# Optimization experiments

Hardware: AMD Instinct MI355X
Metric: run time of the kernel (lower is better)

The kernel has to match this reference:

```python
import jax, jax.numpy as jnp
import numpy as np

APERTURE = 128
LN_EPS = 1e-6

def _layer_norm(y, g, b):
    mu = jnp.mean(y, axis=-1, keepdims=True)
    var = jnp.var(y, axis=-1, keepdims=True)
    return (y - mu) / jnp.sqrt(var + LN_EPS) * g + b

def setup_inputs() -> dict:
    key = jax.random.key(0)
    ks = jax.random.split(key, 12)
    B, S, D = 4, 4096, 1024
    gain = np.sqrt(2.0)
    xav = lambda k, fan_out, fan_in: jax.random.uniform(
        k, (fan_out, fan_in), jnp.float32,
        -gain * np.sqrt(6.0 / (fan_in + fan_out)), gain * np.sqrt(6.0 / (fan_in + fan_out)))
    return {
        "x": jax.random.normal(ks[0], (B, S, D), jnp.float32),
        "Wq": xav(ks[1], D, D),
        "Wk": xav(ks[2], D, D),
        "Wv": xav(ks[3], D, D),
        "Wo": xav(ks[4], D, D),
        "k1_w": xav(ks[5], D, D),
        "k1_b": jnp.full((D,), 0.1, jnp.float32),
        "k2_w": xav(ks[6], 1, D),
        "k2_b": jnp.full((1,), 0.1, jnp.float32),
        "ln_g": jnp.ones((D,), jnp.float32),
        "ln_b": jnp.zeros((D,), jnp.float32),
    }

def reference(x, Wq, Wk, Wv, Wo, k1_w, k1_b, k2_w, k2_b, ln_g, ln_b):
    B, S, D = x.shape
    scale = jnp.float32(1.0 / np.sqrt(D))
    neg_inf = jnp.float32(-np.inf)

    Q = x @ Wq.T  # [B,S,D]
    K = x @ Wk.T
    V = x @ Wv.T

    e = jnp.einsum('bsd,btd->bst', Q, K) * scale  # [B,S,S]

    # ignore_self: -inf on the diagonal
    i = jnp.arange(S)[:, None]
    j = jnp.arange(S)[None, :]
    e = jnp.where(i == j, neg_inf, e)

    # banded aperture mask: tril(e, ap) * triu(e, -ap); zeros of the product -> -inf
    d = j - i
    scope = jnp.where(d <= APERTURE, e, 0.0) * jnp.where(d >= -APERTURE, e, 0.0)
    e = jnp.where(scope == 0.0, neg_inf, e)

    alpha = jax.nn.softmax(e, axis=2)
    c = jnp.einsum('bst,btd->bsd', alpha, V)
    c = c @ Wo.T

    y = c + x
    y = _layer_norm(y, ln_g, ln_b)
    y = jax.nn.relu(y @ k1_w.T + k1_b)
    y = _layer_norm(y, ln_g, ln_b)
    y = jax.nn.sigmoid(y @ k2_w.T + k2_b)  # [B,S,1]
    return y.reshape(B, S)
```

## Files before the change

### kernel.cpp

```cpp
#include <hip/hip_runtime.h>
#include <math.h>

#define DD 1024
#define SS 4096
#define AP 128
#define LN_EPS 1e-6f
#define BK 32
#define BAND 384

typedef __bf16 bf16;
typedef __attribute__((ext_vector_type(4))) __bf16 bf16x4;
typedef __attribute__((ext_vector_type(8))) __bf16 bf16x8;
typedef __attribute__((ext_vector_type(4))) float f32x4;

#define GLOAD_LDS16(g, l)                                                   \
    __builtin_amdgcn_global_load_lds(                                        \
        (const __attribute__((address_space(1))) void*)(g),                  \
        (__attribute__((address_space(3))) void*)(l), 16, 0, 0)

__global__ __launch_bounds__(256) void prep_all(const float* __restrict__ x,
                                                const float* __restrict__ Wq,
                                                const float* __restrict__ Wk,
                                                const float* __restrict__ Wv,
                                                const float* __restrict__ Wo,
                                                const float* __restrict__ k1w,
                                                const float* __restrict__ k1b,
                                                const float* __restrict__ lng,
                                                const float* __restrict__ lnb,
                                                bf16* __restrict__ xb,
                                                bf16* __restrict__ Wob,
                                                bf16* __restrict__ k1g,
                                                bf16* __restrict__ Wtb,
                                                float* __restrict__ u1,
                                                float* __restrict__ c1b) {
    __shared__ float tile[64][65];
    const int bid = blockIdx.x;
    const int tid = threadIdx.x;
    if (bid < 16384) {
        const int i = (bid * 256 + tid) * 4;
        const float4 a = *(const float4*)(x + i);
        bf16x4 o;
        o[0] = (__bf16)a.x; o[1] = (__bf16)a.y; o[2] = (__bf16)a.z; o[3] = (__bf16)a.w;
        *(bf16x4*)(xb + i) = o;
        return;
    }
    if (bid < 18432) {
        const int b2 = bid - 16384;
        const int sel = b2 >> 10;
        const int bb = b2 & 1023;
        const float* s = sel ? k1w : Wo;
        bf16* d = sel ? k1g : Wob;
        const int i = (bb * 256 + tid) * 4;
        float4 a = *(const float4*)(s + i);
        if (sel) {
            const float4 g4 = *(const float4*)(lng + (i & (DD - 1)));
            a.x *= g4.x; a.y *= g4.y; a.z *= g4.z; a.w *= g4.w;
        }
        bf16x4 o;
        o[0] = (__bf16)a.x; o[1] = (__bf16)a.y; o[2] = (__bf16)a.z; o[3] = (__bf16)a.w;
        *(bf16x4*)(d + i) = o;
        return;
    }
    if (bid < 19200) {
        const int t = bid - 18432;
        const int tz = t >> 8;
        const int tb_ = t & 255;
        const float* in = (tz == 0) ? Wq : (tz == 1) ? Wk : Wv;
        bf16* out = Wtb + ((size_t)tz << 20);
        const int r0 = (tb_ >> 4) * 64, c0 = (tb_ & 15) * 64;
        const int lr = tid >> 4;
        const int lc = (tid & 15) * 4;
#pragma unroll
        for (int rr = 0; rr < 4; rr++) {
            const int row = lr + rr * 16;
            const float4 v = *(const float4*)(in + (size_t)(r0 + row) * DD + c0 + lc);
            tile[row][lc] = v.x; tile[row][lc + 1] = v.y;
            tile[row][lc + 2] = v.z; tile[row][lc + 3] = v.w;
        }
        __syncthreads();
#pragma unroll
        for (int rr = 0; rr < 4; rr++) {
            const int row = lr + rr * 16;
            bf16x4 o;
            o[0] = (__bf16)tile[lc + 0][row];
            o[1] = (__bf16)tile[lc + 1][row];
            o[2] = (__bf16)tile[lc + 2][row];
            o[3] = (__bf16)tile[lc + 3][row];
            *(bf16x4*)(out + (size_t)(c0 + row) * DD + r0 + lc) = o;
        }
        return;
    }
    const int pv = bid - 19200;
    const int lane = tid & 63, wave = tid >> 6;
    const int n = pv * 4 + wave;
    const float* row = k1w + (size_t)n * DD + lane * 16;
    float su = 0.f, sb = 0.f;
#pragma unroll
    for (int q = 0; q < 4; q++) {
        const float4 a = *(const float4*)(row + q * 4);
        const float4 g4 = *(const float4*)(lng + lane * 16 + q * 4);
        const float4 b4 = *(const float4*)(lnb + lane * 16 + q * 4);
        su += a.x * g4.x + a.y * g4.y + a.z * g4.z + a.w * g4.w;
        sb += a.x * b4.x + a.y * b4.y + a.z * b4.z + a.w * b4.w;
    }
#pragma unroll
    for (int off = 32; off > 0; off >>= 1) {
        su += __shfl_xor(su, off);
        sb += __shfl_xor(sb, off);
    }
    if (lane == 0) {
        u1[n] = su;
        c1b[n] = sb + k1b[n];
    }
}

__global__ __launch_bounds__(256) void gemm_pair(const bf16* __restrict__ A0,
                                                 const bf16* __restrict__ W0,
                                                 bf16* __restrict__ O0,
                                                 const bf16* __restrict__ A1,
                                                 const bf16* __restrict__ W1,
                                                 bf16* __restrict__ O1) {
    const bf16* A = blockIdx.z ? A1 : A0;
    const bf16* W = blockIdx.z ? W1 : W0;
    bf16* O = blockIdx.z ? O1 : O0;
    __shared__ bf16 As[128 * BK];
    __shared__ bf16 Bs[128 * BK];
    const int tid = threadIdx.x;
    const int lane = tid & 63;
    const int wave = tid >> 6;
    const int wm = wave & 1;
    const int wn = wave >> 1;
    const int m0 = blockIdx.y * 128;
    const int n0 = blockIdx.x * 128;

    const int c = wave * 64 + lane;
    const int ar = c >> 2;
    const int ac = (c & 3) << 3;
    char* AsB = (char*)As;
    char* BsB = (char*)Bs;
    const int lr = lane & 15;
    const int lk = (lane >> 4) << 3;

    f32x4 acc[4][4] = {};

    for (int kt = 0; kt < DD; kt += BK) {
        const bf16* ga0 = A + (size_t)(m0 + ar) * DD + kt + ac;
        const bf16* gb0 = W + (size_t)(n0 + ar) * DD + kt + ac;
        GLOAD_LDS16(ga0, AsB + wave * 1024);
        GLOAD_LDS16(ga0 + (size_t)64 * DD, AsB + 4096 + wave * 1024);
        GLOAD_LDS16(gb0, BsB + wave * 1024);
        GLOAD_LDS16(gb0 + (size_t)64 * DD, BsB + 4096 + wave * 1024);
        __syncthreads();

        bf16x8 af[4], bfr[4];
#pragma unroll
        for (int i = 0; i < 4; i++)
            af[i] = *(const bf16x8*)&As[(wm * 64 + i * 16 + lr) * BK + lk];
#pragma unroll
        for (int j = 0; j < 4; j++)
            bfr[j] = *(const bf16x8*)&Bs[(wn * 64 + j * 16 + lr) * BK + lk];
#pragma unroll
        for (int i = 0; i < 4; i++)
#pragma unroll
            for (int j = 0; j < 4; j++)
                acc[i][j] = __builtin_amdgcn_mfma_f32_16x16x32_bf16(af[i], bfr[j], acc[i][j], 0, 0, 0);
        __syncthreads();
    }

#pragma unroll
    for (int i = 0; i < 4; i++) {
        const int row = m0 + wm * 64 + i * 16 + ((lane >> 4) << 2);
#pragma unroll
        for (int j = 0; j < 4; j++) {
            const int col = n0 + wn * 64 + j * 16 + (lane & 15);
#pragma unroll
            for (int rr = 0; rr < 4; rr++)
                O[(size_t)(row + rr) * DD + col] = (__bf16)acc[i][j][rr];
        }
    }
}


#define KL_STAGE_A(tt, hh, bb)                                               \
    {                                                                        \
        const bf16* gp_ = Aop + gofsA + (tt) * 64 + (hh) * 32;               \
        GLOAD_LDS16(gp_, smem + (bb) + (hh) * 16384 + ldsW);                 \
        GLOAD_LDS16(gp_ + (size_t)128 * DD,                                  \
                    smem + (bb) + (hh) * 16384 + 8192 + ldsW);               \
    }
#define KL_STAGE_B(tt, hh, bb)                                               \
    {                                                                        \
        const bf16* gp_ = Bop + gofsB + (tt) * 64 + (hh) * 32;               \
        GLOAD_LDS16(gp_, smem + (bb) + 32768 + (hh) * 16384 + ldsW);         \
        GLOAD_LDS16(gp_ + (size_t)128 * DD,                                  \
                    smem + (bb) + 32768 + (hh) * 16384 + 8192 + ldsW);       \
    }
#define KL_READS_A(ks, mh)                                                   \
    af[0] = *(const bf16x8*)(sA + bufo + (ks) * 16384 + (mh) * 4096);        \
    af[1] = *(const bf16x8*)(sA + bufo + (ks) * 16384 + (mh) * 4096 + 1024); \
    af[2] = *(const bf16x8*)(sA + bufo + (ks) * 16384 + (mh) * 4096 + 2048); \
    af[3] = *(const bf16x8*)(sA + bufo + (ks) * 16384 + (mh) * 4096 + 3072);
#define KL_READS_B(ks)                                                       \
    bfr[0] = *(const bf16x8*)(sB + bufo + (ks) * 16384);                     \
    bfr[1] = *(const bf16x8*)(sB + bufo + (ks) * 16384 + 1024);              \
    bfr[2] = *(const bf16x8*)(sB + bufo + (ks) * 16384 + 2048);              \
    bfr[3] = *(const bf16x8*)(sB + bufo + (ks) * 16384 + 3072);
#define KL_MFMA4(I, MH)                                                      \
    acc[(MH) * 4 + I][0] = __builtin_amdgcn_mfma_f32_16x16x32_bf16(af[I], bfr[0], acc[(MH) * 4 + I][0], 0, 0, 0); \
    acc[(MH) * 4 + I][1] = __builtin_amdgcn_mfma_f32_16x16x32_bf16(af[I], bfr[1], acc[(MH) * 4 + I][1], 0, 0, 0); \
    acc[(MH) * 4 + I][2] = __builtin_amdgcn_mfma_f32_16x16x32_bf16(af[I], bfr[2], acc[(MH) * 4 + I][2], 0, 0, 0); \
    acc[(MH) * 4 + I][3] = __builtin_amdgcn_mfma_f32_16x16x32_bf16(af[I], bfr[3], acc[(MH) * 4 + I][3], 0, 0, 0);
#define KL_MFMA16(MH)                                                        \
    __builtin_amdgcn_s_setprio(1);                                           \
    KL_MFMA4(0, MH) KL_MFMA4(1, MH) KL_MFMA4(2, MH) KL_MFMA4(3, MH)          \
    __builtin_amdgcn_s_setprio(0);
#define KL_BARRIER(N) asm volatile("s_waitcnt vmcnt(" #N ")\n\ts_barrier" ::: "memory")

__device__ __forceinline__ void kloop256(const bf16* __restrict__ Aop,
                                         const bf16* __restrict__ Bop,
                                         const int m0, const int n0,
                                         char* smem, f32x4 (&acc)[8][4],
                                         const int tid, const int lane,
                                         const int wave, const int wm, const int wn) {
    const int grow = tid >> 2;
    const int gslot = (tid & 3) ^ ((tid >> 3) & 3);
    const size_t gofsA = (size_t)(m0 + grow) * DD + gslot * 8;
    const size_t gofsB = (size_t)(n0 + grow) * DD + gslot * 8;
    const int ldsW = wave * 1024;
    const int sxo = (((lane >> 4) ^ ((lane >> 1) & 3)) << 4);
    const char* sA = smem + wm * 8192 + (lane & 15) * 64 + sxo;
    const char* sB = smem + 32768 + wn * 4096 + (lane & 15) * 64 + sxo;

    bf16x8 af[4], bfr[4];

    KL_STAGE_A(0, 0, 0) KL_STAGE_B(0, 0, 0)
    KL_STAGE_A(0, 1, 0) KL_STAGE_B(0, 1, 0)
    KL_STAGE_A(1, 0, 65536) KL_STAGE_B(1, 0, 65536)

    int bufo = 0;
    for (int t = 0; t < 15; t++) {
        const int nb = bufo ^ 65536;
        KL_BARRIER(8);
        KL_READS_A(0, 0) KL_READS_B(0)
        KL_STAGE_A(t + 1, 1, nb)
        KL_MFMA16(0)
        KL_READS_A(0, 1)
        KL_STAGE_B(t + 1, 1, nb)
        KL_MFMA16(1)
        KL_BARRIER(8);
        KL_READS_A(1, 0) KL_READS_B(1)
        if (t < 14) { KL_STAGE_A(t + 2, 0, bufo) }
        KL_MFMA16(0)
        KL_READS_A(1, 1)
        if (t < 14) { KL_STAGE_B(t + 2, 0, bufo) }
        KL_MFMA16(1)
        bufo = nb;
    }
    KL_BARRIER(4);
    KL_READS_A(0, 0) KL_READS_B(0)
    KL_MFMA16(0)
    KL_READS_A(0, 1)
    KL_MFMA16(1)
    KL_BARRIER(0);
    KL_READS_A(1, 0) KL_READS_B(1)
    KL_MFMA16(0)
    KL_READS_A(1, 1)
    KL_MFMA16(1)
}

__global__ __launch_bounds__(512) void gemm_uv(const bf16* __restrict__ xb,
                                               const bf16* __restrict__ Gt,
                                               const bf16* __restrict__ W2,
                                               bf16* __restrict__ Ub,
                                               bf16* __restrict__ Vt2) {
    __shared__ char smem[131072];
    const int s = blockIdx.x;
    const int half = s >> 8;
    const int sh = s & 255;
    const int p = (sh & 7) | ((sh >> 5) << 3);
    const int q = (sh >> 3) & 3;
    const bf16* A;
    const bf16* W;
    bf16* O;
    int m0, n0;
    size_t ldo;
    if (half == 0) {
        A = xb; W = Gt; O = Ub;
        m0 = p * 256; n0 = q * 256; ldo = DD;
    } else {
        A = W2; W = xb; O = Vt2;
        m0 = q * 256; n0 = p * 256; ldo = (size_t)4 * SS;
    }
    const int tid = threadIdx.x;
    const int lane = tid & 63;
    const int wave = tid >> 6;
    const int wm = wave & 1;
    const int wn = wave >> 1;

    f32x4 acc[8][4] = {};
    kloop256(A, W, m0, n0, smem, acc, tid, lane, wave, wm, wn);

#pragma unroll
    for (int a = 0; a < 8; a++) {
        const int row = m0 + wm * 128 + a * 16 + ((lane >> 4) << 2);
#pragma unroll
        for (int j = 0; j < 4; j++) {
            const int col = n0 + wn * 64 + j * 16 + (lane & 15);
#pragma unroll
            for (int rr = 0; rr < 4; rr++)
                O[(size_t)(row + rr) * ldo + col] = (__bf16)acc[a][j][rr];
        }
    }
}

__global__ __launch_bounds__(512) void gemm_k1(const bf16* __restrict__ T,
                                               const bf16* __restrict__ k1g,
                                               const float* __restrict__ part_t,
                                               const float* __restrict__ u1,
                                               const float* __restrict__ c1b,
                                               const float* __restrict__ lng,
                                               const float* __restrict__ k2w,
                                               float* __restrict__ part_h) {
    __shared__ char smem[131072];
    __shared__ float lmu[256], lrs[256];
    const int m0 = blockIdx.x * 256;
    const int n0 = blockIdx.y * 256;
    const int tid = threadIdx.x;
    const int lane = tid & 63;
    const int wave = tid >> 6;
    const int wm = wave & 1;
    const int wn = wave >> 1;

    if (tid < 256) {
        const float* p = part_t + (size_t)(m0 + tid) * 32;
        float s1 = 0.f, s2 = 0.f;
#pragma unroll
        for (int s = 0; s < 8; s++) {
            const float4 v = *(const float4*)(p + s * 4);
            s1 += v.x + v.z;
            s2 += v.y + v.w;
        }
        const float m = s1 * (1.f / DD);
        lmu[tid] = m;
        lrs[tid] = rsqrtf(s2 * (1.f / DD) - m * m + LN_EPS);
    }
    __syncthreads();

    f32x4 acc[8][4] = {};
    kloop256(T, k1g, m0, n0, smem, acc, tid, lane, wave, wm, wn);

    float u1v[4], cbv[4], ugv[4];
#pragma unroll
    for (int j = 0; j < 4; j++) {
        const int col = n0 + wn * 64 + j * 16 + (lane & 15);
        u1v[j] = u1[col];
        cbv[j] = c1b[col];
        ugv[j] = lng[col] * k2w[col];
    }
    const int strip = blockIdx.y * 4 + wn;
#pragma unroll
    for (int a = 0; a < 8; a++) {
#pragma unroll
        for (int rr = 0; rr < 4; rr++) {
            const int lrow = wm * 128 + a * 16 + ((lane >> 4) << 2) + rr;
            const int row = m0 + lrow;
            const float mr = lmu[lrow], rs = lrs[lrow];
            float s1 = 0.f, s2 = 0.f, s3 = 0.f;
#pragma unroll
            for (int j = 0; j < 4; j++) {
                const float v = rs * (acc[a][j][rr] - mr * u1v[j]) + cbv[j];
                const float h = fmaxf(v, 0.f);
                s1 += h; s2 += h * h; s3 += h * ugv[j];
            }
#pragma unroll
            for (int off = 8; off > 0; off >>= 1) {
                s1 += __shfl_xor(s1, off);
                s2 += __shfl_xor(s2, off);
                s3 += __shfl_xor(s3, off);
            }
            if ((lane & 15) == 0) {
                float* p = part_h + (size_t)row * 48 + strip * 3;
                p[0] = s1; p[1] = s2; p[2] = s3;
            }
        }
    }
}

#define SP_STAGE(tt, bb)                                                      \
    {                                                                         \
        const int kt_ = (tt) * 64;                                            \
        GLOAD_LDS16(U + gofsA + kt_, smem + (bb) + ldsWA);                    \
        GLOAD_LDS16(X + gofsB + kt_, smem + (bb) + 8192 + ldsW);              \
        GLOAD_LDS16(X + gofsB + (long)128 * DD + kt_, smem + (bb) + 16384 + ldsW); \
        GLOAD_LDS16(X + gofsB + (long)256 * DD + kt_, smem + (bb) + 24576 + ldsW); \
        GLOAD_LDS16(X + gofsB + kt_ + 32, smem + (bb) + 32768 + ldsW);        \
        GLOAD_LDS16(X + gofsB + (long)128 * DD + kt_ + 32, smem + (bb) + 40960 + ldsW); \
        GLOAD_LDS16(X + gofsB + (long)256 * DD + kt_ + 32, smem + (bb) + 49152 + ldsW); \
    }
#define SP_READS(bb)                                                          \
    _Pragma("unroll") for (int i_ = 0; i_ < 2; i_++) {                        \
        a0[i_] = *(const bf16x8*)(sA + (bb) + wm * 2048 + i_ * 1024);         \
        a1[i_] = *(const bf16x8*)(sA + (bb) + 4096 + wm * 2048 + i_ * 1024);  \
    }                                                                         \
    _Pragma("unroll") for (int j_ = 0; j_ < 6; j_++) {                        \
        b0[j_] = *(const bf16x8*)(sB + (bb) + wn * 6144 + j_ * 1024);         \
        b1[j_] = *(const bf16x8*)(sB + (bb) + 24576 + wn * 6144 + j_ * 1024); \
    }
#define SP_MFMA(AR, BR)                                                       \
    __builtin_amdgcn_s_setprio(1);                                            \
    _Pragma("unroll") for (int i_ = 0; i_ < 2; i_++)                          \
        _Pragma("unroll") for (int j_ = 0; j_ < 6; j_++)                      \
            acc[i_][j_] = __builtin_amdgcn_mfma_f32_16x16x32_bf16(AR[i_], BR[j_], acc[i_][j_], 0, 0, 0); \
    __builtin_amdgcn_s_setprio(0);
#define SP_LGBAR asm volatile("s_waitcnt lgkmcnt(0)\n\ts_barrier" ::: "memory")

__global__ __launch_bounds__(512) void attn_sp(const bf16* __restrict__ U,
                                               const bf16* __restrict__ X,
                                               bf16* __restrict__ P) {
    __shared__ char smem[114688];
    const int s = blockIdx.x;
    const int t = (s & 7) * 32 + (s >> 3);
    const int tid = threadIdx.x;
    const int lane = tid & 63;
    const int wave = tid >> 6;
    const int wm = wave & 1;
    const int wn = wave >> 1;
    const int m0 = t * 64;
    const long w0 = (long)(t >> 1) * 128 - 128;

    const int grow = tid >> 2;
    const int gslot = (tid & 3) ^ ((tid >> 3) & 3);
    const size_t gofsA = (size_t)(m0 + (grow & 63)) * DD + gslot * 8 + (wave >> 2) * 32;
    const long gofsB = (w0 + grow) * (long)DD + gslot * 8;
    const int ldsWA = (wave & 3) * 1024 + (wave >> 2) * 4096;
    const int ldsW = wave * 1024;
    const int sxo = (((lane >> 4) ^ ((lane >> 1) & 3)) << 4);
    const char* sA = smem + (lane & 15) * 64 + sxo;
    const char* sB = smem + 8192 + (lane & 15) * 64 + sxo;

    f32x4 acc[2][6] = {};
    bf16x8 a0[2], b0[6], a1[2], b1[6];

    SP_STAGE(0, 0)
    SP_STAGE(1, 57344)

#pragma unroll 1
    for (int tt = 0; tt < 14; tt++) {
        const int bb = (tt & 1) * 57344;
        KL_BARRIER(7);
        SP_READS(bb)
        SP_MFMA(a0, b0)
        SP_LGBAR;
        SP_STAGE(tt + 2, bb)
        SP_MFMA(a1, b1)
    }
    KL_BARRIER(7);
    SP_READS(0)
    SP_MFMA(a0, b0)
    SP_MFMA(a1, b1)
    KL_BARRIER(0);
    SP_READS(57344)
    SP_MFMA(a0, b0)
    SP_MFMA(a1, b1)
    __syncthreads();

    float* lredm = (float*)smem;
    float* lreds = lredm + 256;
    const int rbase = wm * 32 + ((lane >> 4) << 2);
    const int ib = (t << 6) & (SS - 1);
    const int jst = ((t >> 1) & 31) * 128 - 128;
    const float scale = 0.03125f;

    float pmx[2][4];
#pragma unroll
    for (int i = 0; i < 2; i++)
#pragma unroll
        for (int rr = 0; rr < 4; rr++) {
            const int irow = ib + rbase + i * 16 + rr;
            float mx = -INFINITY;
#pragma unroll
            for (int j = 0; j < 6; j++) {
                const int jg = jst + wn * 96 + j * 16 + (lane & 15);
                const int dj = jg - irow;
                const bool valid = (jg >= 0) && (jg < SS) && (dj != 0) && (dj <= AP) && (dj >= -AP);
                const float sv = valid ? acc[i][j][rr] * scale : -INFINITY;
                acc[i][j][rr] = sv;
                mx = fmaxf(mx, sv);
            }
#pragma unroll
            for (int off = 8; off > 0; off >>= 1) mx = fmaxf(mx, __shfl_xor(mx, off));
            pmx[i][rr] = mx;
        }
    if ((lane & 15) == 0) {
#pragma unroll
        for (int i = 0; i < 2; i++)
#pragma unroll
            for (int rr = 0; rr < 4; rr++)
                lredm[(rbase + i * 16 + rr) * 4 + wn] = pmx[i][rr];
    }
    __syncthreads();

    float lsum[2][4], mv[2][4];
#pragma unroll
    for (int i = 0; i < 2; i++)
#pragma unroll
        for (int rr = 0; rr < 4; rr++) {
            const int ri = (rbase + i * 16 + rr) * 4;
            mv[i][rr] = fmaxf(fmaxf(lredm[ri], lredm[ri + 1]),
                              fmaxf(lredm[ri + 2], lredm[ri + 3]));
            float su = 0.f;
#pragma unroll
            for (int j = 0; j < 6; j++) {
                const float e = __expf(acc[i][j][rr] - mv[i][rr]);
                acc[i][j][rr] = e;
                su += e;
            }
#pragma unroll
            for (int off = 8; off > 0; off >>= 1) su += __shfl_xor(su, off);
            lsum[i][rr] = su;
        }
    if ((lane & 15) == 0) {
#pragma unroll
        for (int i = 0; i < 2; i++)
#pragma unroll
            for (int rr = 0; rr < 4; rr++)
                lreds[(rbase + i * 16 + rr) * 4 + wn] = lsum[i][rr];
    }
    __syncthreads();

#pragma unroll
    for (int i = 0; i < 2; i++)
#pragma unroll
        for (int rr = 0; rr < 4; rr++) {
            const int ri = (rbase + i * 16 + rr) * 4;
            const float inv = 1.f / (lreds[ri] + lreds[ri + 1] + lreds[ri + 2] + lreds[ri + 3]);
            const size_t ro = (size_t)(m0 + rbase + i * 16 + rr) * BAND;
#pragma unroll
            for (int j = 0; j < 6; j++)
                P[ro + wn * 96 + j * 16 + (lane & 15)] = (__bf16)(acc[i][j][rr] * inv);
        }
}

__global__ __launch_bounds__(512) void attn_pv_mfma(const bf16* __restrict__ P,
                                                    const bf16* __restrict__ Vt,
                                                    const bf16* __restrict__ xres,
                                                    bf16* __restrict__ T,
                                                    float* __restrict__ part_t) {
    __shared__ bf16 As[128 * BK];
    __shared__ bf16 Bs[256 * BK];
    const int tid = threadIdx.x;
    const int lane = tid & 63;
    const int wave = tid >> 6;
    const int wm = wave & 1;
    const int wn = wave >> 1;
    const int t = blockIdx.x;
    const int m0 = t * 128;
    const int n0 = blockIdx.y * 256;
    const bf16* Wb = Vt + (long)t * 128 - 128;

    const int ar = tid >> 2;
    const int ac = (tid & 3) << 3;
    char* AsB = (char*)As;
    char* BsB = (char*)Bs;
    const int lr = lane & 15;
    const int lk = (lane >> 4) << 3;

    f32x4 acc[4][4] = {};

    for (int kt = 0; kt < BAND; kt += BK) {
        const bf16* ga0 = P + (size_t)(m0 + ar) * BAND + kt + ac;
        const bf16* gb0 = Wb + (size_t)(n0 + ar) * (4 * SS) + kt + ac;
        GLOAD_LDS16(ga0, AsB + wave * 1024);
        GLOAD_LDS16(gb0, BsB + wave * 1024);
        GLOAD_LDS16(gb0 + (size_t)128 * (4 * SS), BsB + 8192 + wave * 1024);
        __syncthreads();

        bf16x8 af[4], bfr[4];
#pragma unroll
        for (int i = 0; i < 4; i++)
            af[i] = *(const bf16x8*)&As[(wm * 64 + i * 16 + lr) * BK + lk];
#pragma unroll
        for (int j = 0; j < 4; j++)
            bfr[j] = *(const bf16x8*)&Bs[(wn * 64 + j * 16 + lr) * BK + lk];
#pragma unroll
        for (int i = 0; i < 4; i++)
#pragma unroll
            for (int j = 0; j < 4; j++)
                acc[i][j] = __builtin_amdgcn_mfma_f32_16x16x32_bf16(af[i], bfr[j], acc[i][j], 0, 0, 0);
        __syncthreads();
    }

    const int strip = blockIdx.y * 4 + wn;
#pragma unroll
    for (int i = 0; i < 4; i++) {
#pragma unroll
        for (int rr = 0; rr < 4; rr++) {
            const int row = m0 + wm * 64 + i * 16 + ((lane >> 4) << 2) + rr;
            float s1 = 0.f, s2 = 0.f;
#pragma unroll
            for (int j = 0; j < 4; j++) {
                const int col = n0 + wn * 64 + j * 16 + (lane & 15);
                const size_t idx = (size_t)row * DD + col;
                const __bf16 tv_b = (__bf16)(acc[i][j][rr] + (float)xres[idx]);
                T[idx] = tv_b;
                const float tv = (float)tv_b;
                s1 += tv; s2 += tv * tv;
            }
#pragma unroll
            for (int off = 8; off > 0; off >>= 1) {
                s1 += __shfl_xor(s1, off);
                s2 += __shfl_xor(s2, off);
            }
            if ((lane & 15) == 0) {
                float2 st; st.x = s1; st.y = s2;
                *(float2*)(part_t + (size_t)row * 32 + strip * 2) = st;
            }
        }
    }
}

__global__ __launch_bounds__(256) void ln_k2_p(const float* __restrict__ part_h,
                                               const float* __restrict__ g,
                                               const float* __restrict__ bta,
                                               const float* __restrict__ w2,
                                               const float* __restrict__ b2,
                                               float* __restrict__ out) {
    __shared__ float red[256], red2[256];
    const int tid = threadIdx.x;
    const float4 g4 = *(const float4*)(g + tid * 4);
    const float4 w4 = *(const float4*)(w2 + tid * 4);
    const float4 b4 = *(const float4*)(bta + tid * 4);
    red[tid] = g4.x * w4.x + g4.y * w4.y + g4.z * w4.z + g4.w * w4.w;
    red2[tid] = b4.x * w4.x + b4.y * w4.y + b4.z * w4.z + b4.w * w4.w;
    __syncthreads();
    for (int s = 128; s > 0; s >>= 1) {
        if (tid < s) { red[tid] += red[tid + s]; red2[tid] += red2[tid + s]; }
        __syncthreads();
    }
    const float sum_u = red[0];
    const float sum_bw = red2[0];

    const int r = blockIdx.x * 256 + tid;
    const float* p = part_h + (size_t)r * 48;
    float s1 = 0.f, s2 = 0.f, s3 = 0.f;
#pragma unroll
    for (int s = 0; s < 16; s++) {
        s1 += p[s * 3 + 0];
        s2 += p[s * 3 + 1];
        s3 += p[s * 3 + 2];
    }
    const float m = s1 * (1.f / DD);
    const float var = s2 * (1.f / DD) - m * m;
    const float rs = rsqrtf(var + LN_EPS);
    const float z = rs * (s3 - m * sum_u) + sum_bw + b2[0];
    out[r] = 1.f / (1.f + __expf(-z));
}

extern "C" void kernel_launch(void* const* d_in, const int* in_sizes, int n_in,
                              void* d_out, int out_size, void* d_ws, size_t ws_size,
                              hipStream_t stream) {
    const float* x   = (const float*)d_in[0];
    const float* Wq  = (const float*)d_in[1];
    const float* Wk  = (const float*)d_in[2];
    const float* Wv  = (const float*)d_in[3];
    const float* Wo  = (const float*)d_in[4];
    const float* k1w = (const float*)d_in[5];
    const float* k1b = (const float*)d_in[6];
    const float* k2w = (const float*)d_in[7];
    const float* k2b = (const float*)d_in[8];
    const float* lng = (const float*)d_in[9];
    const float* lnb = (const float*)d_in[10];
    float* out = (float*)d_out;

    const int N = 4 * SS;
    char* ws = (char*)d_ws;
    bf16*  Ub   = (bf16*)(ws);
    bf16*  xb   = (bf16*)(ws + ((size_t)32  << 20));
    bf16*  Vt2  = (bf16*)(ws + ((size_t)64  << 20));
    bf16*  P    = (bf16*)(ws + ((size_t)96  << 20));
    bf16*  T    = (bf16*)(ws + ((size_t)164 << 20));
    bf16*  Wtb  = (bf16*)(ws + ((size_t)196 << 20));
    bf16*  Wqtb = Wtb;
    bf16*  Wktb = Wqtb + (1 << 20);
    bf16*  Wvtb = Wktb + (1 << 20);
    bf16*  Wob  = Wvtb + (1 << 20);
    bf16*  k1g  = Wob  + (1 << 20);
    bf16*  Gtb  = k1g  + (1 << 20);
    bf16*  W2b  = Gtb  + (1 << 20);
    float* u1     = (float*)(ws + ((size_t)210 << 20));
    float* c1b    = u1 + DD;
    float* part_t = (float*)(ws + ((size_t)211 << 20));
    float* part_h = (float*)(ws + ((size_t)214 << 20));

    dim3 tb(256);

    prep_all<<<19456, tb, 0, stream>>>(x, Wq, Wk, Wv, Wo, k1w, k1b, lng, lnb,
                                       xb, Wob, k1g, Wtb, u1, c1b);

    gemm_pair<<<dim3(8, 8, 2), tb, 0, stream>>>(Wktb, Wqtb, Gtb, Wob, Wvtb, W2b);

    gemm_uv<<<512, dim3(512), 0, stream>>>(xb, Gtb, W2b, Ub, Vt2);

    attn_sp<<<256, dim3(512), 0, stream>>>(Ub, xb, P);
    attn_pv_mfma<<<dim3(N / 128, 4), dim3(512), 0, stream>>>(P, Vt2, xb, T, part_t);

    gemm_k1<<<dim3(64, 4), dim3(512), 0, stream>>>(T, k1g, part_t, u1, c1b, lng, k2w, part_h);
    ln_k2_p<<<N / 256, tb, 0, stream>>>(part_h, lng, lnb, k2w, k2b, out);
}
```

Before: 320.5 us.

## Double-buffer PV GEMM with async LDS prefetch and swizzled layout

Rewrites the attention P·V MFMA main loop to use a two-stage LDS ring with BK=64 per stage. The next tile's global-to-LDS loads are issued while MFMAs on the current tile run, and an XOR swizzle is applied to LDS addresses to cut bank conflicts. MFMA sections are wrapped in s_setprio. This uses 96KB of LDS per block, which may limit occupancy, and relies on the existing KL_BARRIER and SP_LGBAR macros being correct for vmcnt waits.

```diff
diff --git a/kernel.cpp b/kernel.cpp
--- a/kernel.cpp
+++ b/kernel.cpp
@@ -541,13 +541,38 @@
         }
 }
 
+#define PV_STAGE(tt, bb)                                                      \
+    {                                                                         \
+        const int kt_ = (tt) * 64;                                            \
+        GLOAD_LDS16(P + gofsP + kt_,        smem + (bb) + ldsW);              \
+        GLOAD_LDS16(P + gofsP + kt_ + 32,   smem + (bb) + 8192 + ldsW);       \
+        GLOAD_LDS16(Wb + gofsV + kt_,       smem + (bb) + 16384 + ldsW);      \
+        GLOAD_LDS16(Wb + gofsV2 + kt_,      smem + (bb) + 24576 + ldsW);      \
+        GLOAD_LDS16(Wb + gofsV + kt_ + 32,  smem + (bb) + 32768 + ldsW);      \
+        GLOAD_LDS16(Wb + gofsV2 + kt_ + 32, smem + (bb) + 40960 + ldsW);      \
+    }
+#define PV_READS(bb)                                                          \
+    _Pragma("unroll") for (int i_ = 0; i_ < 4; i_++) {                        \
+        a0[i_] = *(const bf16x8*)(sA + (bb) + wm * 4096 + i_ * 1024);         \
+        a1[i_] = *(const bf16x8*)(sA + (bb) + 8192 + wm * 4096 + i_ * 1024);  \
+    }                                                                         \
+    _Pragma("unroll") for (int j_ = 0; j_ < 4; j_++) {                        \
+        b0[j_] = *(const bf16x8*)(sB + (bb) + wn * 4096 + j_ * 1024);         \
+        b1[j_] = *(const bf16x8*)(sB + (bb) + 16384 + wn * 4096 + j_ * 1024); \
+    }
+#define PV_MFMA(AR, BR)                                                       \
+    __builtin_amdgcn_s_setprio(1);                                            \
+    _Pragma("unroll") for (int i_ = 0; i_ < 4; i_++)                          \
+        _Pragma("unroll") for (int j_ = 0; j_ < 4; j_++)                      \
+            acc[i_][j_] = __builtin_amdgcn_mfma_f32_16x16x32_bf16(AR[i_], BR[j_], acc[i_][j_], 0, 0, 0); \
+    __builtin_amdgcn_s_setprio(0);
+
 __global__ __launch_bounds__(512) void attn_pv_mfma(const bf16* __restrict__ P,
                                                     const bf16* __restrict__ Vt,
                                                     const bf16* __restrict__ xres,
                                                     bf16* __restrict__ T,
                                                     float* __restrict__ part_t) {
-    __shared__ bf16 As[128 * BK];
-    __shared__ bf16 Bs[256 * BK];
+    __shared__ char smem[98304];
     const int tid = threadIdx.x;
     const int lane = tid & 63;
     const int wave = tid >> 6;
@@ -558,37 +583,40 @@
     const int n0 = blockIdx.y * 256;
     const bf16* Wb = Vt + (long)t * 128 - 128;
 
-    const int ar = tid >> 2;
-    const int ac = (tid & 3) << 3;
-    char* AsB = (char*)As;
-    char* BsB = (char*)Bs;
-    const int lr = lane & 15;
-    const int lk = (lane >> 4) << 3;
+    const int grow = tid >> 2;
+    const int gslot = (tid & 3) ^ ((tid >> 3) & 3);
+    const size_t gofsP = (size_t)(m0 + grow) * BAND + gslot * 8;
+    const size_t gofsV = (size_t)(n0 + grow) * (4 * SS) + gslot * 8;
+    const size_t gofsV2 = gofsV + (size_t)128 * (4 * SS);
+    const int ldsW = wave * 1024;
+    const int sxo = (((lane >> 4) ^ ((lane >> 1) & 3)) << 4);
+    const char* sA = smem + (lane & 15) * 64 + sxo;
+    const char* sB = smem + 16384 + (lane & 15) * 64 + sxo;
 
     f32x4 acc[4][4] = {};
-
-    for (int kt = 0; kt < BAND; kt += BK) {
-        const bf16* ga0 = P + (size_t)(m0 + ar) * BAND + kt + ac;
-        const bf16* gb0 = Wb + (size_t)(n0 + ar) * (4 * SS) + kt + ac;
-        GLOAD_LDS16(ga0, AsB + wave * 1024);
-        GLOAD_LDS16(gb0, BsB + wave * 1024);
-        GLOAD_LDS16(gb0 + (size_t)128 * (4 * SS), BsB + 8192 + wave * 1024);
-        __syncthreads();
-
-        bf16x8 af[4], bfr[4];
-#pragma unroll
-        for (int i = 0; i < 4; i++)
-            af[i] = *(const bf16x8*)&As[(wm * 64 + i * 16 + lr) * BK + lk];
-#pragma unroll
-        for (int j = 0; j < 4; j++)
-            bfr[j] = *(const bf16x8*)&Bs[(wn * 64 + j * 16 + lr) * BK + lk];
-#pragma unroll
-        for (int i = 0; i < 4; i++)
-#pragma unroll
-            for (int j = 0; j < 4; j++)
-                acc[i][j] = __builtin_amdgcn_mfma_f32_16x16x32_bf16(af[i], bfr[j], acc[i][j], 0, 0, 0);
-        __syncthreads();
-    }
+    bf16x8 a0[4], a1[4], b0[4], b1[4];
+
+    PV_STAGE(0, 0)
+    PV_STAGE(1, 49152)
+
+#pragma unroll 1
+    for (int tt = 0; tt < 4; tt++) {
+        const int bb = (tt & 1) * 49152;
+        KL_BARRIER(6);
+        PV_READS(bb)
+        PV_MFMA(a0, b0)
+        SP_LGBAR;
+        PV_STAGE(tt + 2, bb)
+        PV_MFMA(a1, b1)
+    }
+    KL_BARRIER(6);
+    PV_READS(0)
+    PV_MFMA(a0, b0)
+    PV_MFMA(a1, b1)
+    KL_BARRIER(0);
+    PV_READS(49152)
+    PV_MFMA(a0, b0)
+    PV_MFMA(a1, b1)
 
     const int strip = blockIdx.y * 4 + wn;
 #pragma unroll
```

Result: slower. 333.5 us (+4.0%).
